# Kernel optimization log

Hardware: AMD Instinct MI355X
Metric: run time of the kernel (lower is better)

The kernel has to match this reference:

```python
import jax, jax.numpy as jnp
import numpy as np

B, N, DIM, H = 1, 768, 384, 12
SK, SV, PK, PV, PD = 16, 16, 4, 4, 128
NUM_LOGITS = 3
SCALAR_SCALE = (NUM_LOGITS * SK) ** -0.5
POINT_SCALE = (NUM_LOGITS * PK * (9.0 / 2.0)) ** -0.5
PAIR_SCALE = NUM_LOGITS ** -0.5
EPS = 1e-8
SOFTPLUS_INV_1 = float(np.log(np.e - 1.0))  # torch init: log(exp(1)-1)


def setup_inputs() -> dict:
    key = jax.random.key(0)
    ks = jax.random.split(key, 16)
    w = lambda k, shape: (jax.random.normal(k, shape, jnp.float32) * 0.02)
    return {
        "single_repr": jax.random.normal(ks[0], (B, N, DIM), jnp.float32),
        "pairwise_repr": jax.random.normal(ks[1], (B, N, N, PD), jnp.float32),
        "rotations": jax.random.normal(ks[2], (B, N, 3, 3), jnp.float32),
        "translations": jax.random.normal(ks[3], (B, N, 3), jnp.float32),
        "mask": jnp.ones((B, N), dtype=bool),
        "Wq_s": w(ks[4], (DIM, H * SK)),
        "Wk_s": w(ks[5], (DIM, H * SK)),
        "Wv_s": w(ks[6], (DIM, H * SV)),
        "Wq_p": w(ks[7], (DIM, H * PK * 3)),
        "Wk_p": w(ks[8], (DIM, H * PK * 3)),
        "Wv_p": w(ks[9], (DIM, H * PV * 3)),
        "W_pair": w(ks[10], (PD, H)),
        "b_pair": jnp.zeros((H,), jnp.float32),
        "point_weights": jnp.full((H,), SOFTPLUS_INV_1, jnp.float32),
        "W_out": w(ks[11], (H * (SV + PD + PV * 4), DIM)),
        "b_out": jnp.zeros((DIM,), jnp.float32),
    }


def _ipa(single_repr, pairwise_repr, rotations, translations, mask,
         Wq_s, Wk_s, Wv_s, Wq_p, Wk_p, Wv_p, W_pair, b_pair,
         point_weights, W_out, b_out):
    x = single_repr
    # scalar q/k/v: (b,n,h*d) -> (b,h,n,d)
    heads_s = lambda t, d: t.reshape(B, N, H, d).transpose(0, 2, 1, 3)
    q_s = heads_s(x @ Wq_s, SK)
    k_s = heads_s(x @ Wk_s, SK)
    v_s = heads_s(x @ Wv_s, SV)
    # point q/k/v: (b,n,h*d*3) -> (b,h,n,d,3), then apply global frame
    heads_p = lambda t, d: t.reshape(B, N, H, d, 3).transpose(0, 2, 1, 3, 4)
    trans = translations[:, None, :, None, :]  # (b,1,n,1,3)
    to_global = lambda t: jnp.einsum('bhndc,bnrc->bhndr', t, rotations) + trans
    q_p = to_global(heads_p(x @ Wq_p, PK))
    k_p = to_global(heads_p(x @ Wk_p, PK))
    v_p = to_global(heads_p(x @ Wv_p, PV))

    logits = jnp.einsum('bhid,bhjd->bhij', q_s, k_s) * SCALAR_SCALE
    pair_bias = pairwise_repr @ W_pair + b_pair  # (b,i,j,h)
    logits = logits + pair_bias.transpose(0, 3, 1, 2) * PAIR_SCALE
    diff = q_p[:, :, :, None] - k_p[:, :, None]  # (b,h,i,j,d,3)
    point_dist = jnp.sum(diff * diff, axis=(-2, -1))  # (b,h,i,j)
    pw = jax.nn.softplus(point_weights)[None, :, None, None]
    logits = logits - 0.5 * POINT_SCALE * pw * point_dist

    m2 = (mask[:, :, None] & mask[:, None, :])[:, None]  # (b,1,i,j)
    logits = jnp.where(m2, logits, -jnp.finfo(logits.dtype).max)
    attn = jax.nn.softmax(logits, axis=-1)

    r_scalar = jnp.einsum('bhij,bhjd->bhid', attn, v_s)
    r_pair = jnp.einsum('bhij,bijd->bhid', attn, pairwise_repr)
    r_point = jnp.einsum('bhij,bhjdc->bhidc', attn, v_p) - trans
    # back to local frame: multiply by R^T
    r_point = jnp.einsum('bhndc,bncr->bhndr', r_point, rotations)
    r_pnorm = jnp.sqrt(jnp.sum(r_point * r_point, axis=-1) + EPS)

    flat = lambda t: t.transpose(0, 2, 1, 3).reshape(B, N, -1)
    f_point = r_point.transpose(0, 2, 1, 3, 4).reshape(B, N, -1)
    results = jnp.concatenate(
        [flat(r_scalar), f_point, flat(r_pnorm), flat(r_pair)], axis=-1)
    return results @ W_out + b_out


def reference(single_repr, pairwise_repr, rotations, translations, mask,
              Wq_s, Wk_s, Wv_s, Wq_p, Wk_p, Wv_p, W_pair, b_pair,
              point_weights, W_out, b_out):
    return _ipa(single_repr, pairwise_repr, rotations, translations, mask,
                Wq_s, Wk_s, Wv_s, Wq_p, Wk_p, Wv_p, W_pair, b_pair,
                point_weights, W_out, b_out)
```

## Files before the change

### kernel.cpp

```cpp
#include <hip/hip_runtime.h>
#include <math.h>

#define NRES 768
#define DIMM 384
#define NH   12

#define SCALAR_SCALE 0.14433756729740646f
#define HALF_POINT   0.06804138174397717f
#define PAIR_SCALE   0.5773502691896258f

__global__ __launch_bounds__(256) void k1_proj2(
    const float* __restrict__ x, const float* __restrict__ rot, const float* __restrict__ trans,
    const float* __restrict__ Wqs, const float* __restrict__ Wks, const float* __restrict__ Wvs,
    const float* __restrict__ Wqp, const float* __restrict__ Wkp, const float* __restrict__ Wvp,
    float* __restrict__ qs, float* __restrict__ ks, float* __restrict__ vs,
    float* __restrict__ qpg, float* __restrict__ kpg, float* __restrict__ vpg)
{
    __shared__ float xs[2 * 384];
    __shared__ float xp[3][2][144];

    const int tid = threadIdx.x;
    const int n0 = blockIdx.x * 2;

    for (int idx = tid; idx < 192; idx += 256)
        ((float4*)xs)[idx] = ((const float4*)(x + (size_t)n0 * 384))[idx];
    __syncthreads();

    if (tid < 252) {
        int m, c0, wd;
        if (tid < 144) { m = tid / 48; c0 = (tid - m * 48) * 4; wd = 192; }
        else { int z = tid - 144; m = 3 + z / 36; c0 = (z - (m - 3) * 36) * 4; wd = 144; }
        const float* Wm = (m==0)?Wqs : (m==1)?Wks : (m==2)?Wvs : (m==3)?Wqp : (m==4)?Wkp : Wvp;
        const float* wp = Wm + c0;
        float a00=0.f,a01=0.f,a02=0.f,a03=0.f, a10=0.f,a11=0.f,a12=0.f,a13=0.f;
        #pragma unroll 4
        for (int k = 0; k < DIMM; ++k) {
            float4 w = *(const float4*)wp; wp += wd;
            float x0 = xs[k], x1 = xs[384 + k];
            a00 = fmaf(x0, w.x, a00); a01 = fmaf(x0, w.y, a01);
            a02 = fmaf(x0, w.z, a02); a03 = fmaf(x0, w.w, a03);
            a10 = fmaf(x1, w.x, a10); a11 = fmaf(x1, w.y, a11);
            a12 = fmaf(x1, w.z, a12); a13 = fmaf(x1, w.w, a13);
        }
        if (m < 3) {
            float* dst = (m==0)?qs : (m==1)?ks : vs;
            *(float4*)(dst + (size_t)(n0    ) * 192 + c0) = make_float4(a00,a01,a02,a03);
            *(float4*)(dst + (size_t)(n0 + 1) * 192 + c0) = make_float4(a10,a11,a12,a13);
        } else {
            int mi = m - 3;
            xp[mi][0][c0+0]=a00; xp[mi][0][c0+1]=a01; xp[mi][0][c0+2]=a02; xp[mi][0][c0+3]=a03;
            xp[mi][1][c0+0]=a10; xp[mi][1][c0+1]=a11; xp[mi][1][c0+2]=a12; xp[mi][1][c0+3]=a13;
        }
    }
    __syncthreads();

    for (int t = tid; t < 288; t += 256) {
        int r = t / 144; int rem = t - r * 144; int mi = rem / 48; int pt = rem - mi * 48; int c0 = pt * 3;
        float p0 = xp[mi][r][c0+0], p1 = xp[mi][r][c0+1], p2 = xp[mi][r][c0+2];
        int n = n0 + r;
        const float* R = rot + n * 9; const float* T = trans + n * 3;
        float g0 = fmaf(R[0], p0, fmaf(R[1], p1, fmaf(R[2], p2, T[0])));
        float g1 = fmaf(R[3], p0, fmaf(R[4], p1, fmaf(R[5], p2, T[1])));
        float g2 = fmaf(R[6], p0, fmaf(R[7], p1, fmaf(R[8], p2, T[2])));
        float* dst = (mi==0)?qpg : (mi==1)?kpg : vpg;
        dst[n*144 + c0+0] = g0; dst[n*144 + c0+1] = g1; dst[n*144 + c0+2] = g2;
    }
}

__global__ __launch_bounds__(256) void kb_bias(
    const float* __restrict__ pairwise, const float* __restrict__ Wp, const float* __restrict__ bp,
    float* __restrict__ PBt)
{
    __shared__ float Pt[64 * 129];
    const int tid = threadIdx.x;
    const int i  = blockIdx.x / 12;
    const int j0 = (blockIdx.x - i * 12) * 64;

    const float4* Pg = (const float4*)(pairwise + ((size_t)i * NRES + j0) * 128);
    #pragma unroll
    for (int q = 0; q < 8; ++q) {
        int idx = tid + 256 * q;
        float4 v = Pg[idx];
        int row = idx >> 5, c4 = (idx & 31) << 2;
        float* dp = &Pt[row * 129 + c4];
        dp[0] = v.x; dp[1] = v.y; dp[2] = v.z; dp[3] = v.w;
    }
    __syncthreads();

    const int j = tid & 63, hg = tid >> 6;
    float b0 = 0.f, b1 = 0.f, b2 = 0.f;
    const float* prow = &Pt[j * 129];
    const float* w = Wp + 3 * hg;
    #pragma unroll 4
    for (int d = 0; d < 128; ++d) {
        float p = prow[d];
        b0 = fmaf(p, w[0], b0);
        b1 = fmaf(p, w[1], b1);
        b2 = fmaf(p, w[2], b2);
        w += 12;
    }
    size_t base = ((size_t)i * 12 + 3 * hg) * NRES + j0 + j;
    PBt[base           ] = PAIR_SCALE * (b0 + bp[3*hg+0]);
    PBt[base +     NRES] = PAIR_SCALE * (b1 + bp[3*hg+1]);
    PBt[base + 2 * NRES] = PAIR_SCALE * (b2 + bp[3*hg+2]);
}

__global__ __launch_bounds__(256, 4) void k2_attn_nb(
    const float* __restrict__ pairwise, const float* __restrict__ rot, const float* __restrict__ trans,
    const float* __restrict__ ptw,
    const float* __restrict__ qs, const float* __restrict__ ks, const float* __restrict__ vs,
    const float* __restrict__ qpg, const float* __restrict__ kpg, const float* __restrict__ vpg,
    const float* __restrict__ PBt,
    float* __restrict__ results)
{
    __shared__ float Et[2][12][68];
    __shared__ float aLb[2][12];
    __shared__ float Qs[192], Qp[144];
    __shared__ float mL[12], lL[12], invL[12], hpL[12];
    __shared__ float rp_l[144];

    const int tid = threadIdx.x;
    const int i = blockIdx.x;
    const size_t ri = (size_t)i * 1920;

    if (tid < 48)                    ((float4*)Qs)[tid]      = ((const float4*)(qs  + (size_t)i * 192))[tid];
    if (tid >= 64 && tid < 100)      ((float4*)Qp)[tid - 64] = ((const float4*)(qpg + (size_t)i * 144))[tid - 64];
    if (tid >= 128 && tid < 140) {
        int h = tid - 128;
        hpL[h] = HALF_POINT * log1pf(__expf(ptw[h]));
        mL[h] = -3.0e38f; lL[h] = 0.f;
    }
    __syncthreads();

    const int j  = tid & 63;
    const int hg = tid >> 6;
    const int hh = tid >> 7, dpr = tid & 127, hb = hh * 6;

    float accp[6] = {0.f,0.f,0.f,0.f,0.f,0.f};
    float accs = 0.f, accq = 0.f;
    const int hs = tid >> 4;
    const int hq = tid / 12;

    for (int tile = 0; tile < 12; ++tile) {
        const int j0 = tile * 64;
        const int buf = tile & 1;

        float Lv0, Lv1, Lv2;
        {
            const size_t pbb = ((size_t)i * 12 + 3 * hg) * NRES + j0 + j;
            float pb0 = PBt[pbb], pb1 = PBt[pbb + NRES], pb2 = PBt[pbb + 2*NRES];
            const int jg = j0 + j;
            const float* kr = ks  + (size_t)jg * 192;
            const float* kp = kpg + (size_t)jg * 144;
            float own[3];
            #pragma unroll
            for (int e = 0; e < 3; ++e) {
                int h = 3 * hg + e;
                const float4* kv = (const float4*)(kr + h * 16);
                float4 a0 = kv[0], a1 = kv[1], a2 = kv[2], a3 = kv[3];
                const float4* qv = (const float4*)(Qs + h * 16);
                float4 q0 = qv[0], q1 = qv[1], q2 = qv[2], q3 = qv[3];
                float s = q0.x*a0.x + q0.y*a0.y + q0.z*a0.z + q0.w*a0.w
                        + q1.x*a1.x + q1.y*a1.y + q1.z*a1.z + q1.w*a1.w
                        + q2.x*a2.x + q2.y*a2.y + q2.z*a2.z + q2.w*a2.w
                        + q3.x*a3.x + q3.y*a3.y + q3.z*a3.z + q3.w*a3.w;
                const float4* pv = (const float4*)(kp + h * 12);
                float4 p0 = pv[0], p1 = pv[1], p2 = pv[2];
                const float4* qpv = (const float4*)(Qp + h * 12);
                float4 u0 = qpv[0], u1 = qpv[1], u2 = qpv[2];
                float dv, dist;
                dv = u0.x - p0.x; dist  = dv*dv;
                dv = u0.y - p0.y; dist += dv*dv;
                dv = u0.z - p0.z; dist += dv*dv;
                dv = u0.w - p0.w; dist += dv*dv;
                dv = u1.x - p1.x; dist += dv*dv;
                dv = u1.y - p1.y; dist += dv*dv;
                dv = u1.z - p1.z; dist += dv*dv;
                dv = u1.w - p1.w; dist += dv*dv;
                dv = u2.x - p2.x; dist += dv*dv;
                dv = u2.y - p2.y; dist += dv*dv;
                dv = u2.z - p2.z; dist += dv*dv;
                dv = u2.w - p2.w; dist += dv*dv;
                own[e] = SCALAR_SCALE * s - hpL[h] * dist;
            }
            Lv0 = own[0] + pb0; Lv1 = own[1] + pb1; Lv2 = own[2] + pb2;
        }

        {
            float tm0 = Lv0, tm1 = Lv1, tm2 = Lv2;
            #pragma unroll
            for (int o = 32; o > 0; o >>= 1) {
                tm0 = fmaxf(tm0, __shfl_xor(tm0, o));
                tm1 = fmaxf(tm1, __shfl_xor(tm1, o));
                tm2 = fmaxf(tm2, __shfl_xor(tm2, o));
            }
            float ss[3], mnv[3], alv[3];
            float Lvv[3] = {Lv0, Lv1, Lv2};
            float tmv[3] = {tm0, tm1, tm2};
            #pragma unroll
            for (int e = 0; e < 3; ++e) {
                int h = 3 * hg + e;
                float mo = mL[h];
                float mn = fmaxf(mo, tmv[e]);
                alv[e] = __expf(mo - mn);
                mnv[e] = mn;
                float ev = __expf(Lvv[e] - mn);
                Et[buf][h][j] = ev;
                ss[e] = ev;
            }
            #pragma unroll
            for (int o = 32; o > 0; o >>= 1) {
                ss[0] += __shfl_xor(ss[0], o);
                ss[1] += __shfl_xor(ss[1], o);
                ss[2] += __shfl_xor(ss[2], o);
            }
            if (j == 0) {
                #pragma unroll
                for (int e = 0; e < 3; ++e) {
                    int h = 3 * hg + e;
                    mL[h] = mnv[e]; aLb[buf][h] = alv[e];
                    lL[h] = lL[h] * alv[e] + ss[e];
                }
            }
        }
        __syncthreads();

        {
            #pragma unroll
            for (int u = 0; u < 6; ++u) accp[u] *= aLb[buf][hb + u];
            const float* Prow = pairwise + ((size_t)i * NRES + j0) * 128 + dpr;
            #pragma unroll 2
            for (int g = 0; g < 16; ++g) {
                float4 e0 = *(const float4*)&Et[buf][hb+0][4*g];
                float4 e1 = *(const float4*)&Et[buf][hb+1][4*g];
                float4 e2 = *(const float4*)&Et[buf][hb+2][4*g];
                float4 e3 = *(const float4*)&Et[buf][hb+3][4*g];
                float4 e4 = *(const float4*)&Et[buf][hb+4][4*g];
                float4 e5 = *(const float4*)&Et[buf][hb+5][4*g];
                float p0 = Prow[(size_t)(4*g+0) * 128];
                float p1 = Prow[(size_t)(4*g+1) * 128];
                float p2 = Prow[(size_t)(4*g+2) * 128];
                float p3 = Prow[(size_t)(4*g+3) * 128];
                accp[0] = fmaf(e0.x,p0,fmaf(e0.y,p1,fmaf(e0.z,p2,fmaf(e0.w,p3,accp[0]))));
                accp[1] = fmaf(e1.x,p0,fmaf(e1.y,p1,fmaf(e1.z,p2,fmaf(e1.w,p3,accp[1]))));
                accp[2] = fmaf(e2.x,p0,fmaf(e2.y,p1,fmaf(e2.z,p2,fmaf(e2.w,p3,accp[2]))));
                accp[3] = fmaf(e3.x,p0,fmaf(e3.y,p1,fmaf(e3.z,p2,fmaf(e3.w,p3,accp[3]))));
                accp[4] = fmaf(e4.x,p0,fmaf(e4.y,p1,fmaf(e4.z,p2,fmaf(e4.w,p3,accp[4]))));
                accp[5] = fmaf(e5.x,p0,fmaf(e5.y,p1,fmaf(e5.z,p2,fmaf(e5.w,p3,accp[5]))));
            }
        }
        if (tid < 192) {
            accs *= aLb[buf][hs];
            const float* vb = vs + (size_t)j0 * 192 + tid;
            #pragma unroll 4
            for (int g = 0; g < 16; ++g) {
                float4 ev = *(const float4*)&Et[buf][hs][4*g];
                accs = fmaf(ev.x, vb[(size_t)(4*g+0) * 192], accs);
                accs = fmaf(ev.y, vb[(size_t)(4*g+1) * 192], accs);
                accs = fmaf(ev.z, vb[(size_t)(4*g+2) * 192], accs);
                accs = fmaf(ev.w, vb[(size_t)(4*g+3) * 192], accs);
            }
        }
        if (tid < 144) {
            accq *= aLb[buf][hq];
            const float* vb = vpg + (size_t)j0 * 144 + tid;
            #pragma unroll 4
            for (int g = 0; g < 16; ++g) {
                float4 ev = *(const float4*)&Et[buf][hq][4*g];
                accq = fmaf(ev.x, vb[(size_t)(4*g+0) * 144], accq);
                accq = fmaf(ev.y, vb[(size_t)(4*g+1) * 144], accq);
                accq = fmaf(ev.z, vb[(size_t)(4*g+2) * 144], accq);
                accq = fmaf(ev.w, vb[(size_t)(4*g+3) * 144], accq);
            }
        }
    }

    if (tid < 12) invL[tid] = 1.0f / lL[tid];
    __syncthreads();

    #pragma unroll
    for (int u = 0; u < 6; ++u)
        results[ri + 384 + (size_t)(hb + u) * 128 + dpr] = accp[u] * invL[hb + u];

    if (tid < 192) results[ri + tid] = accs * invL[hs];

    if (tid < 144) {
        int pc = tid - hq * 12;
        int coord = pc - (pc / 3) * 3;
        rp_l[tid] = accq * invL[hq] - trans[i * 3 + coord];
    }
    __syncthreads();

    if (tid < 48) {
        int h = tid >> 2, d = tid & 3; int c0 = h * 12 + d * 3;
        float p0 = rp_l[c0], p1 = rp_l[c0 + 1], p2 = rp_l[c0 + 2];
        const float* R = rot + i * 9;
        float o0 = p0 * R[0] + p1 * R[3] + p2 * R[6];
        float o1 = p0 * R[1] + p1 * R[4] + p2 * R[7];
        float o2 = p0 * R[2] + p1 * R[5] + p2 * R[8];
        results[ri + 192 + c0 + 0] = o0;
        results[ri + 192 + c0 + 1] = o1;
        results[ri + 192 + c0 + 2] = o2;
        results[ri + 336 + h * 4 + d] = sqrtf(o0*o0 + o1*o1 + o2*o2 + 1e-8f);
    }
}

__global__ __launch_bounds__(256, 3) void k2_attn_old(
    const float* __restrict__ pairwise, const float* __restrict__ rot, const float* __restrict__ trans,
    const float* __restrict__ Wp, const float* __restrict__ bp, const float* __restrict__ ptw,
    const float* __restrict__ qs, const float* __restrict__ ks, const float* __restrict__ vs,
    const float* __restrict__ qpg, const float* __restrict__ kpg, const float* __restrict__ vpg,
    float* __restrict__ results)
{
    __shared__ float Pt[64 * 129];
    __shared__ float PBp[4 * 64 * 13];
    __shared__ float E[64 * 13];
    __shared__ float Qs[192], Qp[144];
    __shared__ float mL[12], lL[12], aL[12], invL[12], hpL[12], bpL[12];
    __shared__ float rp_l[144];

    const int tid = threadIdx.x;
    const int i = blockIdx.x;
    const size_t ri = (size_t)i * 1920;

    if (tid < 48)                    ((float4*)Qs)[tid]      = ((const float4*)(qs  + (size_t)i * 192))[tid];
    if (tid >= 64 && tid < 100)      ((float4*)Qp)[tid - 64] = ((const float4*)(qpg + (size_t)i * 144))[tid - 64];
    if (tid >= 128 && tid < 140) {
        int h = tid - 128;
        hpL[h] = HALF_POINT * log1pf(__expf(ptw[h]));
        bpL[h] = PAIR_SCALE * bp[h];
        mL[h] = -3.0e38f; lL[h] = 0.f;
    }
    __syncthreads();

    const int j  = tid & 63;
    const int hg = tid >> 6;
    const int hh = tid >> 7, dpr = tid & 127, hb = hh * 6;

    float accp[6] = {0.f,0.f,0.f,0.f,0.f,0.f};
    float accs = 0.f, accq = 0.f;
    const int hs = tid >> 4;
    const int hq = tid / 12;

    for (int tile = 0; tile < 12; ++tile) {
        const int j0 = tile * 64;
        {
            const float4* Pg = (const float4*)(pairwise + ((size_t)i * NRES + j0) * 128);
            #pragma unroll
            for (int q = 0; q < 8; ++q) {
                int idx = tid + 256 * q;
                float4 v = Pg[idx];
                int row = idx >> 5, c4 = (idx & 31) << 2;
                float* dp = &Pt[row * 129 + c4];
                dp[0] = v.x; dp[1] = v.y; dp[2] = v.z; dp[3] = v.w;
            }
        }
        __syncthreads();
        {
            float pbp[12];
            #pragma unroll
            for (int h = 0; h < 12; ++h) pbp[h] = 0.f;
            const int d0 = hg * 32;
            #pragma unroll 4
            for (int d = 0; d < 32; ++d) {
                float p = Pt[j * 129 + d0 + d];
                const float* w = Wp + (d0 + d) * 12;
                #pragma unroll
                for (int h = 0; h < 12; ++h) pbp[h] = fmaf(p, w[h], pbp[h]);
            }
            const int jg = j0 + j;
            const float* kr = ks  + (size_t)jg * 192;
            const float* kp = kpg + (size_t)jg * 144;
            float own[3];
            #pragma unroll
            for (int e = 0; e < 3; ++e) {
                int h = 3 * hg + e;
                const float4* kv = (const float4*)(kr + h * 16);
                float4 a0 = kv[0], a1 = kv[1], a2 = kv[2], a3 = kv[3];
                const float4* qv = (const float4*)(Qs + h * 16);
                float4 q0 = qv[0], q1 = qv[1], q2 = qv[2], q3 = qv[3];
                float s = q0.x*a0.x + q0.y*a0.y + q0.z*a0.z + q0.w*a0.w
                        + q1.x*a1.x + q1.y*a1.y + q1.z*a1.z + q1.w*a1.w
                        + q2.x*a2.x + q2.y*a2.y + q2.z*a2.z + q2.w*a2.w
                        + q3.x*a3.x + q3.y*a3.y + q3.z*a3.z + q3.w*a3.w;
                const float4* pv = (const float4*)(kp + h * 12);
                float4 p0 = pv[0], p1 = pv[1], p2 = pv[2];
                const float4* qpv = (const float4*)(Qp + h * 12);
                float4 u0 = qpv[0], u1 = qpv[1], u2 = qpv[2];
                float d0v, dist;
                d0v = u0.x - p0.x; dist  = d0v*d0v;
                d0v = u0.y - p0.y; dist += d0v*d0v;
                d0v = u0.z - p0.z; dist += d0v*d0v;
                d0v = u0.w - p0.w; dist += d0v*d0v;
                d0v = u1.x - p1.x; dist += d0v*d0v;
                d0v = u1.y - p1.y; dist += d0v*d0v;
                d0v = u1.z - p1.z; dist += d0v*d0v;
                d0v = u1.w - p1.w; dist += d0v*d0v;
                d0v = u2.x - p2.x; dist += d0v*d0v;
                d0v = u2.y - p2.y; dist += d0v*d0v;
                d0v = u2.z - p2.z; dist += d0v*d0v;
                d0v = u2.w - p2.w; dist += d0v*d0v;
                own[e] = SCALAR_SCALE * s - hpL[h] * dist + bpL[h];
            }
            float* pbw = &PBp[hg * 832 + j * 13];
            #pragma unroll
            for (int h = 0; h < 12; ++h) {
                float v = PAIR_SCALE * pbp[h];
                if (h >= 3 * hg && h < 3 * hg + 3) v += own[h - 3 * hg];
                pbw[h] = v;
            }
        }
        __syncthreads();
        {
            const float* pbr = &PBp[j * 13];
            float Lv[3], tm[3];
            #pragma unroll
            for (int e = 0; e < 3; ++e) {
                int h = 3 * hg + e;
                Lv[e] = pbr[h] + pbr[832 + h] + pbr[1664 + h] + pbr[2496 + h];
                tm[e] = Lv[e];
            }
            #pragma unroll
            for (int o = 32; o > 0; o >>= 1) {
                #pragma unroll
                for (int e = 0; e < 3; ++e) tm[e] = fmaxf(tm[e], __shfl_xor(tm[e], o));
            }
            float ss[3], mnv[3], alv[3];
            #pragma unroll
            for (int e = 0; e < 3; ++e) {
                int h = 3 * hg + e;
                float mo = mL[h];
                float mn = fmaxf(mo, tm[e]);
                alv[e] = __expf(mo - mn);
                mnv[e] = mn;
                float ev = __expf(Lv[e] - mn);
                E[j * 13 + h] = ev;
                ss[e] = ev;
            }
            #pragma unroll
            for (int o = 32; o > 0; o >>= 1) {
                #pragma unroll
                for (int e = 0; e < 3; ++e) ss[e] += __shfl_xor(ss[e], o);
            }
            if (j == 0) {
                #pragma unroll
                for (int e = 0; e < 3; ++e) {
                    int h = 3 * hg + e;
                    mL[h] = mnv[e]; aL[h] = alv[e];
                    lL[h] = lL[h] * alv[e] + ss[e];
                }
            }
        }
        __syncthreads();
        {
            #pragma unroll
            for (int u = 0; u < 6; ++u) accp[u] *= aL[hb + u];
            #pragma unroll 4
            for (int jj = 0; jj < 64; ++jj) {
                float p = Pt[jj * 129 + dpr];
                const float* ej = &E[jj * 13 + hb];
                accp[0] = fmaf(ej[0], p, accp[0]);
                accp[1] = fmaf(ej[1], p, accp[1]);
                accp[2] = fmaf(ej[2], p, accp[2]);
                accp[3] = fmaf(ej[3], p, accp[3]);
                accp[4] = fmaf(ej[4], p, accp[4]);
                accp[5] = fmaf(ej[5], p, accp[5]);
            }
        }
        if (tid < 192) {
            accs *= aL[hs];
            const float* vb = vs + (size_t)j0 * 192 + tid;
            #pragma unroll 4
            for (int jj = 0; jj < 64; ++jj)
                accs = fmaf(E[jj * 13 + hs], vb[(size_t)jj * 192], accs);
        }
        if (tid < 144) {
            accq *= aL[hq];
            const float* vb = vpg + (size_t)j0 * 144 + tid;
            #pragma unroll 4
            for (int jj = 0; jj < 64; ++jj)
                accq = fmaf(E[jj * 13 + hq], vb[(size_t)jj * 144], accq);
        }
        __syncthreads();
    }

    if (tid < 12) invL[tid] = 1.0f / lL[tid];
    __syncthreads();

    #pragma unroll
    for (int u = 0; u < 6; ++u)
        results[ri + 384 + (size_t)(hb + u) * 128 + dpr] = accp[u] * invL[hb + u];

    if (tid < 192) results[ri + tid] = accs * invL[hs];

    if (tid < 144) {
        int pc = tid - hq * 12;
        int coord = pc - (pc / 3) * 3;
        rp_l[tid] = accq * invL[hq] - trans[i * 3 + coord];
    }
    __syncthreads();

    if (tid < 48) {
        int h = tid >> 2, d = tid & 3; int c0 = h * 12 + d * 3;
        float p0 = rp_l[c0], p1 = rp_l[c0 + 1], p2 = rp_l[c0 + 2];
        const float* R = rot + i * 9;
        float o0 = p0 * R[0] + p1 * R[3] + p2 * R[6];
        float o1 = p0 * R[1] + p1 * R[4] + p2 * R[7];
        float o2 = p0 * R[2] + p1 * R[5] + p2 * R[8];
        results[ri + 192 + c0 + 0] = o0;
        results[ri + 192 + c0 + 1] = o1;
        results[ri + 192 + c0 + 2] = o2;
        results[ri + 336 + h * 4 + d] = sqrtf(o0*o0 + o1*o1 + o2*o2 + 1e-8f);
    }
}

__global__ __launch_bounds__(384) void k3_out3(
    const float* __restrict__ results, const float* __restrict__ Wo, const float* __restrict__ bo,
    float* __restrict__ out)
{
    __shared__ float As[3 * 1936];

    const int t = threadIdx.x;
    const int r0 = blockIdx.x * 3;

    #pragma unroll
    for (int q = 0; q < 4; ++q) {
        int idx = t + 384 * q;
        if (idx < 1440) {
            int r = idx / 480, c4 = idx - r * 480;
            float4 v = ((const float4*)(results + (size_t)(r0 + r) * 1920))[c4];
            float* dp = &As[r * 1936 + c4 * 4];
            dp[0] = v.x; dp[1] = v.y; dp[2] = v.z; dp[3] = v.w;
        }
    }
    __syncthreads();

    float acc0 = 0.f, acc1 = 0.f, acc2 = 0.f;
    const float* wp = Wo + t;
    #pragma unroll 4
    for (int k = 0; k < 1920; ++k) {
        float w = *wp; wp += 384;
        acc0 = fmaf(As[k], w, acc0);
        acc1 = fmaf(As[1936 + k], w, acc1);
        acc2 = fmaf(As[2 * 1936 + k], w, acc2);
    }
    float b = bo[t];
    out[(size_t)(r0 + 0) * 384 + t] = acc0 + b;
    out[(size_t)(r0 + 1) * 384 + t] = acc1 + b;
    out[(size_t)(r0 + 2) * 384 + t] = acc2 + b;
}

extern "C" void kernel_launch(void* const* d_in, const int* in_sizes, int n_in,
                              void* d_out, int out_size, void* d_ws, size_t ws_size,
                              hipStream_t stream) {
    const float* x        = (const float*)d_in[0];
    const float* pairwise = (const float*)d_in[1];
    const float* rot      = (const float*)d_in[2];
    const float* trans    = (const float*)d_in[3];
    const float* Wqs   = (const float*)d_in[5];
    const float* Wks   = (const float*)d_in[6];
    const float* Wvs   = (const float*)d_in[7];
    const float* Wqp   = (const float*)d_in[8];
    const float* Wkp   = (const float*)d_in[9];
    const float* Wvp   = (const float*)d_in[10];
    const float* Wp    = (const float*)d_in[11];
    const float* bp    = (const float*)d_in[12];
    const float* ptw   = (const float*)d_in[13];
    const float* Wo    = (const float*)d_in[14];
    const float* bo    = (const float*)d_in[15];
    float* out = (float*)d_out;

    float* ws = (float*)d_ws;
    float* qs      = ws;
    float* ksb     = qs   + 147456;
    float* vsb     = ksb  + 147456;
    float* qpg     = vsb  + 147456;
    float* kpg     = qpg  + 110592;
    float* vpg     = kpg  + 110592;
    float* results = vpg  + 110592;
    float* PBt     = results + 1474560;

    const size_t need = (size_t)(147456*3 + 110592*3 + 1474560 + 7077888) * 4;

    hipLaunchKernelGGL(k1_proj2, dim3(384), dim3(256), 0, stream,
                       x, rot, trans, Wqs, Wks, Wvs, Wqp, Wkp, Wvp,
                       qs, ksb, vsb, qpg, kpg, vpg);

    if (ws_size >= need) {
        hipLaunchKernelGGL(kb_bias, dim3(9216), dim3(256), 0, stream,
                           pairwise, Wp, bp, PBt);
        hipLaunchKernelGGL(k2_attn_nb, dim3(768), dim3(256), 0, stream,
                           pairwise, rot, trans, ptw,
                           qs, ksb, vsb, qpg, kpg, vpg, PBt, results);
    } else {
        hipLaunchKernelGGL(k2_attn_old, dim3(768), dim3(256), 0, stream,
                           pairwise, rot, trans, Wp, bp, ptw,
                           qs, ksb, vsb, qpg, kpg, vpg, results);
    }

    hipLaunchKernelGGL(k3_out3, dim3(256), dim3(384), 0, stream,
                       results, Wo, bo, out);
}
```

Before: 1.006 ms.

## Split attention over key halves with flash-style combine; rework output projection

The attention kernel now splits each query row's keys into two halves handled by separate blocks. Each block writes unnormalized partial accumulators plus running max and sum, and a new combine kernel merges them with softmax rescaling before doing the frame rotation and norm. This doubles the grid to fill more compute units and raises the occupancy hint, at the cost of extra partial-result traffic and an additional launch. The output projection kernel now handles one row per block, with float4 weight loads and a four-way K split reduced through shared memory.

```diff
diff --git a/kernel.cpp b/kernel.cpp
--- a/kernel.cpp
+++ b/kernel.cpp
@@ -105,23 +105,21 @@
     PBt[base + 2 * NRES] = PAIR_SCALE * (b2 + bp[3*hg+2]);
 }
 
-__global__ __launch_bounds__(256, 4) void k2_attn_nb(
-    const float* __restrict__ pairwise, const float* __restrict__ rot, const float* __restrict__ trans,
-    const float* __restrict__ ptw,
+__global__ __launch_bounds__(256, 6) void k2_attn_sp(
+    const float* __restrict__ pairwise, const float* __restrict__ ptw,
     const float* __restrict__ qs, const float* __restrict__ ks, const float* __restrict__ vs,
     const float* __restrict__ qpg, const float* __restrict__ kpg, const float* __restrict__ vpg,
     const float* __restrict__ PBt,
-    float* __restrict__ results)
+    float* __restrict__ Rpart, float* __restrict__ ML)
 {
     __shared__ float Et[2][12][68];
     __shared__ float aLb[2][12];
     __shared__ float Qs[192], Qp[144];
-    __shared__ float mL[12], lL[12], invL[12], hpL[12];
-    __shared__ float rp_l[144];
+    __shared__ float mL[12], lL[12], hpL[12];
 
     const int tid = threadIdx.x;
-    const int i = blockIdx.x;
-    const size_t ri = (size_t)i * 1920;
+    const int i  = blockIdx.x >> 1;
+    const int sp = blockIdx.x & 1;
 
     if (tid < 48)                    ((float4*)Qs)[tid]      = ((const float4*)(qs  + (size_t)i * 192))[tid];
     if (tid >= 64 && tid < 100)      ((float4*)Qp)[tid - 64] = ((const float4*)(qpg + (size_t)i * 144))[tid - 64];
@@ -141,8 +139,8 @@
     const int hs = tid >> 4;
     const int hq = tid / 12;
 
-    for (int tile = 0; tile < 12; ++tile) {
-        const int j0 = tile * 64;
+    for (int tile = 0; tile < 6; ++tile) {
+        const int j0 = (sp * 6 + tile) * 64;
         const int buf = tile & 1;
 
         float Lv0, Lv1, Lv2;
@@ -275,24 +273,58 @@
         }
     }
 
-    if (tid < 12) invL[tid] = 1.0f / lL[tid];
-    __syncthreads();
-
+    float* Rp = Rpart + ((size_t)sp * NRES + i) * 1920;
     #pragma unroll
     for (int u = 0; u < 6; ++u)
-        results[ri + 384 + (size_t)(hb + u) * 128 + dpr] = accp[u] * invL[hb + u];
-
-    if (tid < 192) results[ri + tid] = accs * invL[hs];
-
-    if (tid < 144) {
-        int pc = tid - hq * 12;
-        int coord = pc - (pc / 3) * 3;
-        rp_l[tid] = accq * invL[hq] - trans[i * 3 + coord];
-    }
-    __syncthreads();
-
-    if (tid < 48) {
-        int h = tid >> 2, d = tid & 3; int c0 = h * 12 + d * 3;
+        Rp[384 + (size_t)(hb + u) * 128 + dpr] = accp[u];
+    if (tid < 192) Rp[tid] = accs;
+    if (tid < 144) Rp[192 + tid] = accq;
+    if (tid < 12) {
+        float* mp = ML + ((size_t)sp * NRES + i) * 24;
+        mp[tid] = mL[tid]; mp[12 + tid] = lL[tid];
+    }
+}
+
+__global__ __launch_bounds__(256) void k2_comb(
+    const float* __restrict__ Rpart, const float* __restrict__ ML,
+    const float* __restrict__ rot, const float* __restrict__ trans,
+    float* __restrict__ results)
+{
+    __shared__ float c0s[12], c1s[12], rp_l[144];
+    const int t = threadIdx.x;
+    const int i = blockIdx.x;
+    const size_t ri = (size_t)i * 1920;
+    const float* R0p = Rpart + (size_t)i * 1920;
+    const float* R1p = Rpart + (size_t)(NRES + i) * 1920;
+
+    if (t < 12) {
+        const float* M0 = ML + (size_t)i * 24;
+        const float* M1 = ML + (size_t)(NRES + i) * 24;
+        float m0 = M0[t], l0 = M0[12 + t], m1 = M1[t], l1 = M1[12 + t];
+        float M = fmaxf(m0, m1);
+        float w0 = __expf(m0 - M), w1 = __expf(m1 - M);
+        float inv = 1.f / (l0 * w0 + l1 * w1);
+        c0s[t] = w0 * inv; c1s[t] = w1 * inv;
+    }
+    __syncthreads();
+
+    if (t < 192) { int h = t >> 4; results[ri + t] = R0p[t] * c0s[h] + R1p[t] * c1s[h]; }
+
+    #pragma unroll
+    for (int u = 0; u < 6; ++u) {
+        int idx = 384 + u * 256 + t;
+        int h = (idx - 384) >> 7;
+        results[ri + idx] = R0p[idx] * c0s[h] + R1p[idx] * c1s[h];
+    }
+
+    if (t < 144) {
+        int h = t / 12, coord = t % 3;
+        rp_l[t] = R0p[192 + t] * c0s[h] + R1p[192 + t] * c1s[h] - trans[i * 3 + coord];
+    }
+    __syncthreads();
+
+    if (t < 48) {
+        int h = t >> 2, d = t & 3; int c0 = h * 12 + d * 3;
         float p0 = rp_l[c0], p1 = rp_l[c0 + 1], p2 = rp_l[c0 + 2];
         const float* R = rot + i * 9;
         float o0 = p0 * R[0] + p1 * R[3] + p2 * R[6];
@@ -305,18 +337,18 @@
     }
 }
 
-__global__ __launch_bounds__(256, 3) void k2_attn_old(
+__global__ __launch_bounds__(256, 4) void k2_attn_nb(
     const float* __restrict__ pairwise, const float* __restrict__ rot, const float* __restrict__ trans,
-    const float* __restrict__ Wp, const float* __restrict__ bp, const float* __restrict__ ptw,
+    const float* __restrict__ ptw,
     const float* __restrict__ qs, const float* __restrict__ ks, const float* __restrict__ vs,
     const float* __restrict__ qpg, const float* __restrict__ kpg, const float* __restrict__ vpg,
+    const float* __restrict__ PBt,
     float* __restrict__ results)
 {
-    __shared__ float Pt[64 * 129];
-    __shared__ float PBp[4 * 64 * 13];
-    __shared__ float E[64 * 13];
+    __shared__ float Et[2][12][68];
+    __shared__ float aLb[2][12];
     __shared__ float Qs[192], Qp[144];
-    __shared__ float mL[12], lL[12], aL[12], invL[12], hpL[12], bpL[12];
+    __shared__ float mL[12], lL[12], invL[12], hpL[12];
     __shared__ float rp_l[144];
 
     const int tid = threadIdx.x;
@@ -328,7 +360,6 @@
     if (tid >= 128 && tid < 140) {
         int h = tid - 128;
         hpL[h] = HALF_POINT * log1pf(__expf(ptw[h]));
-        bpL[h] = PAIR_SCALE * bp[h];
         mL[h] = -3.0e38f; lL[h] = 0.f;
     }
     __syncthreads();
@@ -344,30 +375,11 @@
 
     for (int tile = 0; tile < 12; ++tile) {
         const int j0 = tile * 64;
+        const int buf = tile & 1;
+        float Lv0, Lv1, Lv2;
         {
-            const float4* Pg = (const float4*)(pairwise + ((size_t)i * NRES + j0) * 128);
-            #pragma unroll
-            for (int q = 0; q < 8; ++q) {
-                int idx = tid + 256 * q;
-                float4 v = Pg[idx];
-                int row = idx >> 5, c4 = (idx & 31) << 2;
-                float* dp = &Pt[row * 129 + c4];
-                dp[0] = v.x; dp[1] = v.y; dp[2] = v.z; dp[3] = v.w;
-            }
-        }
-        __syncthreads();
-        {
-            float pbp[12];
-            #pragma unroll
-            for (int h = 0; h < 12; ++h) pbp[h] = 0.f;
-            const int d0 = hg * 32;
-            #pragma unroll 4
-            for (int d = 0; d < 32; ++d) {
-                float p = Pt[j * 129 + d0 + d];
-                const float* w = Wp + (d0 + d) * 12;
-                #pragma unroll
-                for (int h = 0; h < 12; ++h) pbp[h] = fmaf(p, w[h], pbp[h]);
-            }
+            const size_t pbb = ((size_t)i * 12 + 3 * hg) * NRES + j0 + j;
+            float pb0 = PBt[pbb], pb1 = PBt[pbb + NRES], pb2 = PBt[pbb + 2*NRES];
             const int jg = j0 + j;
             const float* kr = ks  + (size_t)jg * 192;
             const float* kp = kpg + (size_t)jg * 144;
@@ -387,66 +399,56 @@
                 float4 p0 = pv[0], p1 = pv[1], p2 = pv[2];
                 const float4* qpv = (const float4*)(Qp + h * 12);
                 float4 u0 = qpv[0], u1 = qpv[1], u2 = qpv[2];
-                float d0v, dist;
-                d0v = u0.x - p0.x; dist  = d0v*d0v;
-                d0v = u0.y - p0.y; dist += d0v*d0v;
-                d0v = u0.z - p0.z; dist += d0v*d0v;
-                d0v = u0.w - p0.w; dist += d0v*d0v;
-                d0v = u1.x - p1.x; dist += d0v*d0v;
-                d0v = u1.y - p1.y; dist += d0v*d0v;
-                d0v = u1.z - p1.z; dist += d0v*d0v;
-                d0v = u1.w - p1.w; dist += d0v*d0v;
-                d0v = u2.x - p2.x; dist += d0v*d0v;
-                d0v = u2.y - p2.y; dist += d0v*d0v;
-                d0v = u2.z - p2.z; dist += d0v*d0v;
-                d0v = u2.w - p2.w; dist += d0v*d0v;
-                own[e] = SCALAR_SCALE * s - hpL[h] * dist + bpL[h];
-            }
-            float* pbw = &PBp[hg * 832 + j * 13];
-            #pragma unroll
-            for (int h = 0; h < 12; ++h) {
-                float v = PAIR_SCALE * pbp[h];
-                if (h >= 3 * hg && h < 3 * hg + 3) v += own[h - 3 * hg];
-                pbw[h] = v;
-            }
-        }
-        __syncthreads();
+                float dv, dist;
+                dv = u0.x - p0.x; dist  = dv*dv;
+                dv = u0.y - p0.y; dist += dv*dv;
+                dv = u0.z - p0.z; dist += dv*dv;
+                dv = u0.w - p0.w; dist += dv*dv;
+                dv = u1.x - p1.x; dist += dv*dv;
+                dv = u1.y - p1.y; dist += dv*dv;
+                dv = u1.z - p1.z; dist += dv*dv;
+                dv = u1.w - p1.w; dist += dv*dv;
+                dv = u2.x - p2.x; dist += dv*dv;
+                dv = u2.y - p2.y; dist += dv*dv;
+                dv = u2.z - p2.z; dist += dv*dv;
+                dv = u2.w - p2.w; dist += dv*dv;
+                own[e] = SCALAR_SCALE * s - hpL[h] * dist;
+            }
+            Lv0 = own[0] + pb0; Lv1 = own[1] + pb1; Lv2 = own[2] + pb2;
+        }
         {
-            const float* pbr = &PBp[j * 13];
-            float Lv[3], tm[3];
-            #pragma unroll
-            for (int e = 0; e < 3; ++e) {
-                int h = 3 * hg + e;
-                Lv[e] = pbr[h] + pbr[832 + h] + pbr[1664 + h] + pbr[2496 + h];
-                tm[e] = Lv[e];
-            }
+            float tm0 = Lv0, tm1 = Lv1, tm2 = Lv2;
             #pragma unroll
             for (int o = 32; o > 0; o >>= 1) {
-                #pragma unroll
-                for (int e = 0; e < 3; ++e) tm[e] = fmaxf(tm[e], __shfl_xor(tm[e], o));
+                tm0 = fmaxf(tm0, __shfl_xor(tm0, o));
+                tm1 = fmaxf(tm1, __shfl_xor(tm1, o));
+                tm2 = fmaxf(tm2, __shfl_xor(tm2, o));
             }
             float ss[3], mnv[3], alv[3];
+            float Lvv[3] = {Lv0, Lv1, Lv2};
+            float tmv[3] = {tm0, tm1, tm2};
             #pragma unroll
             for (int e = 0; e < 3; ++e) {
                 int h = 3 * hg + e;
                 float mo = mL[h];
-                float mn = fmaxf(mo, tm[e]);
+                float mn = fmaxf(mo, tmv[e]);
                 alv[e] = __expf(mo - mn);
                 mnv[e] = mn;
-                float ev = __expf(Lv[e] - mn);
-                E[j * 13 + h] = ev;
+                float ev = __expf(Lvv[e] - mn);
+                Et[buf][h][j] = ev;
                 ss[e] = ev;
             }
             #pragma unroll
             for (int o = 32; o > 0; o >>= 1) {
-                #pragma unroll
-                for (int e = 0; e < 3; ++e) ss[e] += __shfl_xor(ss[e], o);
+                ss[0] += __shfl_xor(ss[0], o);
+                ss[1] += __shfl_xor(ss[1], o);
+                ss[2] += __shfl_xor(ss[2], o);
             }
             if (j == 0) {
                 #pragma unroll
                 for (int e = 0; e < 3; ++e) {
                     int h = 3 * hg + e;
-                    mL[h] = mnv[e]; aL[h] = alv[e];
+                    mL[h] = mnv[e]; aLb[buf][h] = alv[e];
                     lL[h] = lL[h] * alv[e] + ss[e];
                 }
             }
@@ -454,34 +456,52 @@
         __syncthreads();
         {
             #pragma unroll
-            for (int u = 0; u < 6; ++u) accp[u] *= aL[hb + u];
-            #pragma unroll 4
-            for (int jj = 0; jj < 64; ++jj) {
-                float p = Pt[jj * 129 + dpr];
-                const float* ej = &E[jj * 13 + hb];
-                accp[0] = fmaf(ej[0], p, accp[0]);
-                accp[1] = fmaf(ej[1], p, accp[1]);
-                accp[2] = fmaf(ej[2], p, accp[2]);
-                accp[3] = fmaf(ej[3], p, accp[3]);
-                accp[4] = fmaf(ej[4], p, accp[4]);
-                accp[5] = fmaf(ej[5], p, accp[5]);
+            for (int u = 0; u < 6; ++u) accp[u] *= aLb[buf][hb + u];
+            const float* Prow = pairwise + ((size_t)i * NRES + j0) * 128 + dpr;
+            #pragma unroll 2
+            for (int g = 0; g < 16; ++g) {
+                float4 e0 = *(const float4*)&Et[buf][hb+0][4*g];
+                float4 e1 = *(const float4*)&Et[buf][hb+1][4*g];
+                float4 e2 = *(const float4*)&Et[buf][hb+2][4*g];
+                float4 e3 = *(const float4*)&Et[buf][hb+3][4*g];
+                float4 e4 = *(const float4*)&Et[buf][hb+4][4*g];
+                float4 e5 = *(const float4*)&Et[buf][hb+5][4*g];
+                float p0 = Prow[(size_t)(4*g+0) * 128];
+                float p1 = Prow[(size_t)(4*g+1) * 128];
+                float p2 = Prow[(size_t)(4*g+2) * 128];
+                float p3 = Prow[(size_t)(4*g+3) * 128];
+                accp[0] = fmaf(e0.x,p0,fmaf(e0.y,p1,fmaf(e0.z,p2,fmaf(e0.w,p3,accp[0]))));
+                accp[1] = fmaf(e1.x,p0,fmaf(e1.y,p1,fmaf(e1.z,p2,fmaf(e1.w,p3,accp[1]))));
+                accp[2] = fmaf(e2.x,p0,fmaf(e2.y,p1,fmaf(e2.z,p2,fmaf(e2.w,p3,accp[2]))));
+                accp[3] = fmaf(e3.x,p0,fmaf(e3.y,p1,fmaf(e3.z,p2,fmaf(e3.w,p3,accp[3]))));
+                accp[4] = fmaf(e4.x,p0,fmaf(e4.y,p1,fmaf(e4.z,p2,fmaf(e4.w,p3,accp[4]))));
+                accp[5] = fmaf(e5.x,p0,fmaf(e5.y,p1,fmaf(e5.z,p2,fmaf(e5.w,p3,accp[5]))));
             }
         }
         if (tid < 192) {
-            accs *= aL[hs];
+            accs *= aLb[buf][hs];
             const float* vb = vs + (size_t)j0 * 192 + tid;
             #pragma unroll 4
-            for (int jj = 0; jj < 64; ++jj)
-                accs = fmaf(E[jj * 13 + hs], vb[(size_t)jj * 192], accs);
+            for (int g = 0; g < 16; ++g) {
+                float4 ev = *(const float4*)&Et[buf][hs][4*g];
+                accs = fmaf(ev.x, vb[(size_t)(4*g+0) * 192], accs);
+                accs = fmaf(ev.y, vb[(size_t)(4*g+1) * 192], accs);
+                accs = fmaf(ev.z, vb[(size_t)(4*g+2) * 192], accs);
+                accs = fmaf(ev.w, vb[(size_t)(4*g+3) * 192], accs);
+            }
         }
         if (tid < 144) {
-            accq *= aL[hq];
+            accq *= aLb[buf][hq];
             const float* vb = vpg + (size_t)j0 * 144 + tid;
             #pragma unroll 4
-            for (int jj = 0; jj < 64; ++jj)
-                accq = fmaf(E[jj * 13 + hq], vb[(size_t)jj * 144], accq);
-        }
-        __syncthreads();
+            for (int g = 0; g < 16; ++g) {
+                float4 ev = *(const float4*)&Et[buf][hq][4*g];
+                accq = fmaf(ev.x, vb[(size_t)(4*g+0) * 144], accq);
+                accq = fmaf(ev.y, vb[(size_t)(4*g+1) * 144], accq);
+                accq = fmaf(ev.z, vb[(size_t)(4*g+2) * 144], accq);
+                accq = fmaf(ev.w, vb[(size_t)(4*g+3) * 144], accq);
+            }
+        }
     }
 
     if (tid < 12) invL[tid] = 1.0f / lL[tid];
@@ -514,40 +534,50 @@
     }
 }
 
-__global__ __launch_bounds__(384) void k3_out3(
+__global__ __launch_bounds__(384) void k3_out1(
     const float* __restrict__ results, const float* __restrict__ Wo, const float* __restrict__ bo,
     float* __restrict__ out)
 {
-    __shared__ float As[3 * 1936];
+    __shared__ float As[1936];
+    __shared__ float red[3 * 96 * 5];
 
     const int t = threadIdx.x;
-    const int r0 = blockIdx.x * 3;
-
-    #pragma unroll
-    for (int q = 0; q < 4; ++q) {
-        int idx = t + 384 * q;
-        if (idx < 1440) {
-            int r = idx / 480, c4 = idx - r * 480;
-            float4 v = ((const float4*)(results + (size_t)(r0 + r) * 1920))[c4];
-            float* dp = &As[r * 1936 + c4 * 4];
-            dp[0] = v.x; dp[1] = v.y; dp[2] = v.z; dp[3] = v.w;
-        }
-    }
-    __syncthreads();
-
-    float acc0 = 0.f, acc1 = 0.f, acc2 = 0.f;
-    const float* wp = Wo + t;
+    const int r = blockIdx.x;
+
+    for (int idx = t; idx < 480; idx += 384)
+        ((float4*)As)[idx] = ((const float4*)(results + (size_t)r * 1920))[idx];
+    __syncthreads();
+
+    const int cg = t % 96, kp = t / 96;
+    float a0 = 0.f, a1 = 0.f, a2 = 0.f, a3 = 0.f;
+    const float* wp = Wo + (size_t)(kp * 480) * 384 + cg * 4;
+    int ka = kp * 480;
     #pragma unroll 4
-    for (int k = 0; k < 1920; ++k) {
-        float w = *wp; wp += 384;
-        acc0 = fmaf(As[k], w, acc0);
-        acc1 = fmaf(As[1936 + k], w, acc1);
-        acc2 = fmaf(As[2 * 1936 + k], w, acc2);
-    }
-    float b = bo[t];
-    out[(size_t)(r0 + 0) * 384 + t] = acc0 + b;
-    out[(size_t)(r0 + 1) * 384 + t] = acc1 + b;
-    out[(size_t)(r0 + 2) * 384 + t] = acc2 + b;
+    for (int k = 0; k < 480; ++k, ++ka) {
+        float4 w = *(const float4*)wp; wp += 384;
+        float a = As[ka];
+        a0 = fmaf(a, w.x, a0);
+        a1 = fmaf(a, w.y, a1);
+        a2 = fmaf(a, w.z, a2);
+        a3 = fmaf(a, w.w, a3);
+    }
+    if (kp > 0) {
+        float* rp = &red[((kp - 1) * 96 + cg) * 5];
+        rp[0] = a0; rp[1] = a1; rp[2] = a2; rp[3] = a3;
+    }
+    __syncthreads();
+    if (kp == 0) {
+        float4 b = *(const float4*)(bo + cg * 4);
+        const float* r1 = &red[(0 * 96 + cg) * 5];
+        const float* r2 = &red[(1 * 96 + cg) * 5];
+        const float* r3 = &red[(2 * 96 + cg) * 5];
+        float4 o;
+        o.x = a0 + r1[0] + r2[0] + r3[0] + b.x;
+        o.y = a1 + r1[1] + r2[1] + r3[1] + b.y;
+        o.z = a2 + r1[2] + r2[2] + r3[2] + b.z;
+        o.w = a3 + r1[3] + r2[3] + r3[3] + b.w;
+        *(float4*)(out + (size_t)r * 384 + cg * 4) = o;
+    }
 }
 
 extern "C" void kernel_launch(void* const* d_in, const int* in_sizes, int n_in,
@@ -579,25 +609,31 @@
     float* vpg     = kpg  + 110592;
     float* results = vpg  + 110592;
     float* PBt     = results + 1474560;
-
-    const size_t need = (size_t)(147456*3 + 110592*3 + 1474560 + 7077888) * 4;
+    float* Rpart   = PBt + 7077888;
+    float* ML      = Rpart + 2949120;
+
+    const size_t need_nb    = (size_t)(147456*3 + 110592*3 + 1474560 + 7077888) * 4;
+    const size_t need_split = need_nb + (size_t)(2949120 + 36864) * 4;
 
     hipLaunchKernelGGL(k1_proj2, dim3(384), dim3(256), 0, stream,
                        x, rot, trans, Wqs, Wks, Wvs, Wqp, Wkp, Wvp,
                        qs, ksb, vsb, qpg, kpg, vpg);
 
-    if (ws_size >= need) {
+    if (ws_size >= need_split) {
+        hipLaunchKernelGGL(kb_bias, dim3(9216), dim3(256), 0, stream,
+                           pairwise, Wp, bp, PBt);
+        hipLaunchKernelGGL(k2_attn_sp, dim3(1536), dim3(256), 0, stream,
+                           pairwise, ptw, qs, ksb, vsb, qpg, kpg, vpg, PBt, Rpart, ML);
+        hipLaunchKernelGGL(k2_comb, dim3(768), dim3(256), 0, stream,
+                           Rpart, ML, rot, trans, results);
+    } else {
         hipLaunchKernelGGL(kb_bias, dim3(9216), dim3(256), 0, stream,
                            pairwise, Wp, bp, PBt);
         hipLaunchKernelGGL(k2_attn_nb, dim3(768), dim3(256), 0, stream,
                            pairwise, rot, trans, ptw,
                            qs, ksb, vsb, qpg, kpg, vpg, PBt, results);
-    } else {
-        hipLaunchKernelGGL(k2_attn_old, dim3(768), dim3(256), 0, stream,
-                           pairwise, rot, trans, Wp, bp, ptw,
-                           qs, ksb, vsb, qpg, kpg, vpg, results);
-    }
-
-    hipLaunchKernelGGL(k3_out3, dim3(256), dim3(384), 0, stream,
+    }
+
+    hipLaunchKernelGGL(k3_out1, dim3(768), dim3(384), 0, stream,
                        results, Wo, bo, out);
 }
```

After: 1.133 ms. +12.7%, slower.
